# Optimization experiments

Hardware: AMD Instinct MI355X
Metric: run time of the kernel (lower is better)

## Reference

```python
import jax, jax.numpy as jnp
import numpy as np

N, E, IN_FEATS, D, H, DIST_DIM, NBOUND = 10000, 160000, 128, 64, 4, 32, 31

def setup_inputs() -> dict:
    key = jax.random.key(0)
    ks = jax.random.split(key, 16)
    gain = 5.0 / 3.0  # tanh gain
    def xavier(k, shape):
        # xavier_normal over the last two dims (fan_in, fan_out) as torch does per-slice
        fan_in, fan_out = shape[-2], shape[-1]
        std = gain * np.sqrt(2.0 / (fan_in + fan_out))
        return jax.random.normal(k, shape, dtype=jnp.float32) * std
    inp = {
        'feat': jax.random.normal(ks[0], (N, IN_FEATS), dtype=jnp.float32),
        'locations': jax.random.normal(ks[1], (N, 3), dtype=jnp.float32),
        'src': jax.random.randint(ks[2], (E,), 0, N),
        'dst': jax.random.randint(ks[3], (E,), 0, N),
        'inter_ids': jax.random.randint(ks[4], (E, H), 0, N),
        'W_fc': xavier(ks[5], (IN_FEATS, H * D)),
        'embed_table': jax.random.normal(ks[6], (NBOUND + 1, DIST_DIM), dtype=jnp.float32),
        'G': xavier(ks[7], (H, DIST_DIM, D)),
        'attn_fc1': xavier(ks[8], (H, 2 * D, D)),
        'attn_fc2': xavier(ks[9], (H, 2 * D, D)),
        'attn_fc3': xavier(ks[10], (H, 2 * D, D)),
        'attn_fc': xavier(ks[11], (H, 3 * D, D)),
        'attn_out': xavier(ks[12], (H, D, 1)),
        'boundaries': jnp.linspace(0.1, 3.1, NBOUND).astype(jnp.float32),
    }
    return inp


def reference(feat, locations, W_fc, embed_table, G, attn_fc1, attn_fc2, attn_fc3,
              attn_fc, attn_out, boundaries, src, dst, inter_ids):
    n = feat.shape[0]
    h = (feat @ W_fc).reshape(n, H, D)                      # [N,H,D]
    pos = locations                                          # [N,3]
    src_pos = pos[src]                                       # [E,3]
    dst_pos = pos[dst]                                       # [E,3]
    inter_pos = pos[inter_ids]                               # [E,H,3]
    h_src = h[src]                                           # [E,H,D]
    h_dst = h[dst]                                           # [E,H,D]
    head_idx = jnp.arange(H)[None, :]
    inter_h = h[inter_ids, head_idx, :]                      # [E,H,D] per-head gather

    e_count = src.shape[0]
    dist1 = jnp.broadcast_to(jnp.linalg.norm(dst_pos - src_pos, axis=-1)[:, None], (e_count, H))
    dist2 = jnp.linalg.norm(dst_pos[:, None, :] - inter_pos, axis=-1)   # [E,H]
    dist_ = jnp.linalg.norm(src_pos[:, None, :] - inter_pos, axis=-1)   # [E,H]

    def dist_embed(dist):
        idx = jnp.searchsorted(boundaries, dist, side='left')  # torch.bucketize(right=False)
        e = embed_table[idx]                                   # [E,H,DIST_DIM]
        return jnp.einsum('ehk,hkd->ehd', e, G)                # [E,H,D]

    de1 = dist_embed(dist1)
    de2 = dist_embed(dist2)
    de_ = dist_embed(dist_)

    d1 = jnp.einsum('ehk,hkd->ehd', jnp.concatenate([h_src, de1], axis=-1), attn_fc1)
    d2 = jnp.einsum('ehk,hkd->ehd', jnp.concatenate([inter_h, de2], axis=-1), attn_fc2)
    d3 = jnp.einsum('ehk,hkd->ehd', jnp.concatenate([h_dst, de_], axis=-1), attn_fc3)

    h_c = jnp.tanh(jnp.einsum('ehk,hkd->ehd', jnp.concatenate([d1, d2, d3], axis=-1), attn_fc))
    e_score = jnp.einsum('ehd,hdo->eho', h_c, attn_out)[..., 0]        # [E,H]

    # edge softmax grouped by destination node
    m = jax.ops.segment_max(e_score, dst, num_segments=n)              # [N,H]
    ex = jnp.exp(e_score - m[dst])
    den = jax.ops.segment_sum(ex, dst, num_segments=n)                 # [N,H]
    a = ex / den[dst]                                                  # [E,H]

    ft = jax.ops.segment_sum(a[:, :, None] * h_src, dst, num_segments=n)  # [N,H,D]
    rst = jnp.mean(ft, axis=1)                                          # merge='mean' -> [N,D]
    return rst
```

## Files before the change

### kernel.cpp

```cpp
#include <hip/hip_runtime.h>
#include <hip/hip_fp16.h>
#include <math.h>

#define N_NODES 10000
#define E_EDGES 160000
#define DMODEL 64
#define H 4
#define NBOUND 31
#define SLOTS 64
#define QREC 1024

typedef _Float16 half8 __attribute__((ext_vector_type(8)));
typedef float floatx4 __attribute__((ext_vector_type(4)));

__device__ __forceinline__ void mm4(const float* __restrict__ S, int aoff,
                                    int astride, int boff, int i0, int j,
                                    int Kdim, float o[4]) {
  float a0 = 0.f, a1 = 0.f, a2 = 0.f, a3 = 0.f;
  for (int t4 = 0; t4 < (Kdim >> 2); ++t4) {
    float4 f0 = *(const float4*)&S[aoff + (i0 + 0) * astride + t4 * 4];
    float4 f1 = *(const float4*)&S[aoff + (i0 + 1) * astride + t4 * 4];
    float4 f2 = *(const float4*)&S[aoff + (i0 + 2) * astride + t4 * 4];
    float4 f3 = *(const float4*)&S[aoff + (i0 + 3) * astride + t4 * 4];
    float b0 = S[boff + (t4 * 4 + 0) * 64 + j];
    float b1 = S[boff + (t4 * 4 + 1) * 64 + j];
    float b2 = S[boff + (t4 * 4 + 2) * 64 + j];
    float b3 = S[boff + (t4 * 4 + 3) * 64 + j];
    a0 += f0.x * b0 + f0.y * b1 + f0.z * b2 + f0.w * b3;
    a1 += f1.x * b0 + f1.y * b1 + f1.z * b2 + f1.w * b3;
    a2 += f2.x * b0 + f2.y * b1 + f2.z * b2 + f2.w * b3;
    a3 += f3.x * b0 + f3.y * b1 + f3.z * b2 + f3.w * b3;
  }
  o[0] = a0; o[1] = a1; o[2] = a2; o[3] = a3;
}

__device__ __forceinline__ int didx(const float* __restrict__ bnd2, float d) {
  int g = (int)(d * 10.0f);
  g = (g < 0) ? 0 : ((g > 31) ? 31 : g);
  g += (bnd2[g + 1] < d) ? 1 : 0;
  g -= (bnd2[g] >= d) ? 1 : 0;
  return g;
}

__global__ __launch_bounds__(512) void prep_kernel(
    const float* __restrict__ fc1, const float* __restrict__ fc2,
    const float* __restrict__ fc3, const float* __restrict__ fcc,
    const float* __restrict__ Wfc, const float* __restrict__ G,
    const float* __restrict__ emb, const float* __restrict__ pos,
    __half* __restrict__ bigWT, __half* __restrict__ U16,
    int* __restrict__ cnt, float4* __restrict__ pos4) {
  __shared__ __align__(16) float S[12288];
  int bi = blockIdx.x;
  int tid = threadIdx.x;
  if (bi >= 36) {
    int n = (bi - 36) * 512 + tid;
    if (n < N_NODES) {
      cnt[n] = 0;
      pos4[n] = make_float4(pos[n * 3], pos[n * 3 + 1], pos[n * 3 + 2], 0.f);
    }
    return;
  }
  int ca = bi / 12;
  int kh = bi % 12;
  int k = kh >> 2, h = kh & 3;
  const float* fck = (k == 0) ? fc1 : (k == 1) ? fc2 : fc3;
  fck += h * 128 * 64;
  const float* F = fcc + h * 192 * 64 + k * 64 * 64;
  int j = tid & 63, ig = tid >> 6;
  float o[4];
  if (ca < 2) {
    #pragma unroll
    for (int u = 0; u < 2; ++u) {
      ((float4*)S)[u * 512 + tid] = ((const float4*)F)[u * 512 + tid];
      ((float4*)(S + 4096))[u * 512 + tid] = ((const float4*)fck)[u * 512 + tid];
    }
    __syncthreads();
    #pragma unroll
    for (int rg = 0; rg < 2; ++rg) {
      int i0 = ig * 8 + rg * 4;
      mm4(S, 4096, 64, 0, i0, j, 64, o);
      S[8192 + (i0 + 0) * 64 + j] = o[0];
      S[8192 + (i0 + 1) * 64 + j] = o[1];
      S[8192 + (i0 + 2) * 64 + j] = o[2];
      S[8192 + (i0 + 3) * 64 + j] = o[3];
    }
    __syncthreads();
    int rbase = (ca == 0) ? 0 : 64;
    #pragma unroll
    for (int u = 0; u < 2; ++u) {
      int fi = u * 512 + tid;
      int i = fi >> 4, c4 = fi & 15;
      ((float4*)(S + 4096))[fi] =
          ((const float4*)(Wfc + (rbase + i) * 256 + h * 64))[c4];
    }
    __syncthreads();
    if (k == 0) {
      #pragma unroll
      for (int u = 0; u < 8; ++u) {
        int idx = u * 512 + tid;
        int i = idx >> 6, jj = idx & 63;
        bigWT[(h * 64 + jj) * 128 + rbase + i] = __float2half(S[4096 + idx]);
      }
    }
    #pragma unroll
    for (int rg = 0; rg < 2; ++rg) {
      int i0 = ig * 8 + rg * 4;
      mm4(S, 4096, 64, 8192, i0, j, 64, o);
      int rb = ((k + 1) * 256 + h * 64 + j) * 128 + rbase;
      bigWT[rb + i0 + 0] = __float2half(o[0]);
      bigWT[rb + i0 + 1] = __float2half(o[1]);
      bigWT[rb + i0 + 2] = __float2half(o[2]);
      bigWT[rb + i0 + 3] = __float2half(o[3]);
    }
    return;
  }
  #pragma unroll
  for (int u = 0; u < 2; ++u) {
    ((float4*)S)[u * 512 + tid] = ((const float4*)F)[u * 512 + tid];
    ((float4*)(S + 4096))[u * 512 + tid] =
        ((const float4*)(fck + 4096))[u * 512 + tid];
  }
  __syncthreads();
  #pragma unroll
  for (int rg = 0; rg < 2; ++rg) {
    int i0 = ig * 8 + rg * 4;
    mm4(S, 4096, 64, 0, i0, j, 64, o);
    S[8192 + (i0 + 0) * 64 + j] = o[0];
    S[8192 + (i0 + 1) * 64 + j] = o[1];
    S[8192 + (i0 + 2) * 64 + j] = o[2];
    S[8192 + (i0 + 3) * 64 + j] = o[3];
  }
  __syncthreads();
  ((float4*)S)[tid] = ((const float4*)(G + h * 2048))[tid];
  if (tid < 256) ((float4*)(S + 2048))[tid] = ((const float4*)emb)[tid];
  __syncthreads();
  {
    int i0 = ig * 4;
    mm4(S, 0, 64, 8192, i0, j, 64, o);
    S[3072 + (i0 + 0) * 64 + j] = o[0];
    S[3072 + (i0 + 1) * 64 + j] = o[1];
    S[3072 + (i0 + 2) * 64 + j] = o[2];
    S[3072 + (i0 + 3) * 64 + j] = o[3];
  }
  __syncthreads();
  {
    int i0 = ig * 4;
    mm4(S, 2048, 32, 3072, i0, j, 32, o);
    int base = k * 8192 + h * 2048;
    U16[base + (i0 + 0) * 64 + j] = __float2half(o[0]);
    U16[base + (i0 + 1) * 64 + j] = __float2half(o[1]);
    U16[base + (i0 + 2) * 64 + j] = __float2half(o[2]);
    U16[base + (i0 + 3) * 64 + j] = __float2half(o[3]);
  }
}

#define EROW 264
#define NEDGE_BLK 1250

__global__ __launch_bounds__(128) void gemm_edge_kernel(
    const float* __restrict__ feat, const __half* __restrict__ bigWT,
    __half* __restrict__ qall, const float4* __restrict__ pos4,
    const int* __restrict__ src, const int* __restrict__ dst,
    const int* __restrict__ inter, const float* __restrict__ boundaries,
    int* __restrict__ cnt, uint4* __restrict__ ebuf) {
  __shared__ __align__(16) __half Esm[2][16][EROW];
  __shared__ float Sb[48];
  int bi = blockIdx.x;
  int tid = threadIdx.x;
  if (bi < NEDGE_BLK) {
    if (tid < NBOUND) Sb[tid + 1] = boundaries[tid];
    if (tid == NBOUND) { Sb[0] = -INFINITY; Sb[32] = INFINITY; }
    __syncthreads();
    int e = bi * 128 + tid;
    int s = src[e], t = dst[e];
    int4 iv = *(const int4*)&inter[e * 4];
    int itarr[4] = {iv.x, iv.y, iv.z, iv.w};
    float4 sp = pos4[s];
    float4 tp = pos4[t];
    float dx = tp.x - sp.x, dy = tp.y - sp.y, dz = tp.z - sp.z;
    float dist1 = sqrtf(dx * dx + dy * dy + dz * dz);
    unsigned i1 = (unsigned)didx(Sb, dist1);
    unsigned w3 = 0, q20 = 0, q_0 = 0;
    #pragma unroll
    for (int hh = 0; hh < 4; ++hh) {
      float4 ip = pos4[itarr[hh]];
      float ax = tp.x - ip.x, ay = tp.y - ip.y, az = tp.z - ip.z;
      float dist2 = sqrtf(ax * ax + ay * ay + az * az);
      float bx = sp.x - ip.x, by = sp.y - ip.y, bz = sp.z - ip.z;
      float dist_ = sqrtf(bx * bx + by * by + bz * bz);
      unsigned idx2 = (unsigned)didx(Sb, dist2);
      unsigned idx_ = (unsigned)didx(Sb, dist_);
      if (hh == 0) { q20 = idx2; q_0 = idx_; }
      else w3 |= (idx2 | (idx_ << 5)) << ((hh - 1) * 10);
    }
    uint4 rec;
    rec.x = (unsigned)s | ((unsigned)itarr[0] << 16);
    rec.y = (unsigned)itarr[1] | ((unsigned)itarr[2] << 16);
    rec.z = (unsigned)itarr[3] | (i1 << 16) | (q20 << 21) | (q_0 << 26);
    rec.w = w3;
    int p = atomicAdd(&cnt[t], 1);
    if (p < SLOTS) ebuf[t * SLOTS + p] = rec;
    return;
  }
  int gi = bi - NEDGE_BLK;
  int bx = gi % 313, by = gi / 313;
  int wv = tid >> 6, l = tid & 63;
  int m0 = bx * 32 + wv * 16;
  int n0 = by * 256;
  int lm = l & 15, lk = (l >> 4) * 8;
  int arow = m0 + lm;
  if (arow >= N_NODES) arow = N_NODES - 1;
  const float* fp = feat + arow * 128 + lk;
  const _Float16* bp = (const _Float16*)bigWT + lk;
  half8 a[4];
  #pragma unroll
  for (int kt = 0; kt < 4; ++kt) {
    float4 u0 = *(const float4*)(fp + kt * 32);
    float4 u1 = *(const float4*)(fp + kt * 32 + 4);
    half8 t;
    t[0] = (_Float16)u0.x; t[1] = (_Float16)u0.y;
    t[2] = (_Float16)u0.z; t[3] = (_Float16)u0.w;
    t[4] = (_Float16)u1.x; t[5] = (_Float16)u1.y;
    t[6] = (_Float16)u1.z; t[7] = (_Float16)u1.w;
    a[kt] = t;
  }
  #pragma unroll
  for (int nt = 0; nt < 16; ++nt) {
    floatx4 acc = (floatx4){0.f, 0.f, 0.f, 0.f};
    #pragma unroll
    for (int kt = 0; kt < 4; ++kt) {
      half8 b = *(const half8*)(bp + (n0 + nt * 16 + lm) * 128 + kt * 32);
      acc = __builtin_amdgcn_mfma_f32_16x16x32_f16(a[kt], b, acc, 0, 0, 0);
    }
    int dd = nt * 16 + lm;
    #pragma unroll
    for (int r4 = 0; r4 < 4; ++r4)
      Esm[wv][(l >> 4) * 4 + r4][dd] = __float2half(acc[r4]);
  }
  __syncthreads();
  int row = l >> 2;
  int j0 = (l & 3) * 64;
  int m = m0 + row;
  if (m < N_NODES) {
    #pragma unroll
    for (int u = 0; u < 8; ++u) {
      uint4 v = *(const uint4*)&Esm[wv][row][j0 + u * 8];
      *(uint4*)&qall[m * QREC + by * 256 + j0 + u * 8] = v;
    }
  }
}

__device__ __forceinline__ float dpp_bfly_sum16(float v) {
  int x;
  x = __builtin_amdgcn_update_dpp(0, __float_as_int(v), 0xB1, 0xf, 0xf, true);
  v += __int_as_float(x);
  x = __builtin_amdgcn_update_dpp(0, __float_as_int(v), 0x4E, 0xf, 0xf, true);
  v += __int_as_float(x);
  x = __builtin_amdgcn_update_dpp(0, __float_as_int(v), 0x141, 0xf, 0xf, true);
  v += __int_as_float(x);
  x = __builtin_amdgcn_update_dpp(0, __float_as_int(v), 0x140, 0xf, 0xf, true);
  v += __int_as_float(x);
  return v;
}

union H4u { uint2 u; __half2 h[2]; };

__device__ __forceinline__ float tanh_dot(H4u A, H4u B, H4u C, H4u X, H4u Y,
                                          H4u Z, float4 a4) {
  __half2 z0 = __hadd2(__hadd2(A.h[0], B.h[0]), __hadd2(C.h[0], X.h[0]));
  z0 = __hadd2(z0, __hadd2(Y.h[0], Z.h[0]));
  __half2 z1 = __hadd2(__hadd2(A.h[1], B.h[1]), __hadd2(C.h[1], X.h[1]));
  z1 = __hadd2(z1, __hadd2(Y.h[1], Z.h[1]));
  float2 f0 = __half22float2(z0);
  float2 f1 = __half22float2(z1);
  const float K = 2.885390082f;
  float p0 = __builtin_amdgcn_exp2f(f0.x * K);
  float p1 = __builtin_amdgcn_exp2f(f0.y * K);
  float p2 = __builtin_amdgcn_exp2f(f1.x * K);
  float p3 = __builtin_amdgcn_exp2f(f1.y * K);
  float r0 = __builtin_amdgcn_rcpf(p0 + 1.0f);
  float r1 = __builtin_amdgcn_rcpf(p1 + 1.0f);
  float r2 = __builtin_amdgcn_rcpf(p2 + 1.0f);
  float r3 = __builtin_amdgcn_rcpf(p3 + 1.0f);
  float dot = a4.x * r0;
  dot = fmaf(a4.y, r1, dot);
  dot = fmaf(a4.z, r2, dot);
  dot = fmaf(a4.w, r3, dot);
  float asum = (a4.x + a4.y) + (a4.z + a4.w);
  return fmaf(-2.0f, dot, asum);
}

__device__ __forceinline__ float4 h4_to_f4(uint2 u) {
  union { uint2 ui; __half2 h[2]; } cc;
  cc.ui = u;
  float2 a = __half22float2(cc.h[0]);
  float2 b = __half22float2(cc.h[1]);
  return make_float4(a.x, a.y, b.x, b.y);
}

__device__ __forceinline__ void dec_rec(uint4 r, int h, int* s, int* it,
                                        unsigned* i1, unsigned* q2,
                                        unsigned* q_) {
  *s = (int)(r.x & 0xffff);
  *it = (h == 0) ? (int)(r.x >> 16)
      : (h == 1) ? (int)(r.y & 0xffff)
      : (h == 2) ? (int)(r.y >> 16) : (int)(r.z & 0xffff);
  *i1 = (r.z >> 16) & 31;
  if (h == 0) {
    *q2 = (r.z >> 21) & 31;
    *q_ = (r.z >> 26) & 31;
  } else {
    unsigned f = r.w >> ((h - 1) * 10);
    *q2 = f & 31;
    *q_ = (f >> 5) & 31;
  }
}

__global__ __launch_bounds__(256) void score_agg_kernel(
    const int* __restrict__ cnt, const uint4* __restrict__ ebuf,
    const __half* __restrict__ qall, const __half* __restrict__ U16,
    const float* __restrict__ aout, float* __restrict__ out) {
  __shared__ uint4 recs[SLOTS];
  __shared__ float4 sm_num[4][64];
  __shared__ float sm_den[4][4];
  int tid = threadIdx.x;
  int w = tid >> 6, lane = tid & 63;
  int h = lane >> 4, c = lane & 15;
  int n = blockIdx.x;
  int deg = cnt[n];
  if (deg > SLOTS) deg = SLOTS;
  if (tid < deg) recs[tid] = ebuf[n * SLOTS + tid];
  H4u C;
  C.u = *(const uint2*)(qall + n * QREC + 768 + h * 64 + c * 4);
  const float4 a4 = *((const float4*)(aout + h * 64) + c);
  __syncthreads();
  float4 num = make_float4(0.f, 0.f, 0.f, 0.f);
  float den = 0.f;
  int hc4 = h * 64 + c * 4;
  for (int i = w; i < deg; i += 8) {
    int iB = i + 4;
    int vB = (iB < deg);
    uint4 rA = recs[i];
    uint4 rB = recs[vB ? iB : i];
    int sA, itA, sB, itB;
    unsigned i1A, q2A, q_A, i1B, q2B, q_B;
    dec_rec(rA, h, &sA, &itA, &i1A, &q2A, &q_A);
    dec_rec(rB, h, &sB, &itB, &i1B, &q2B, &q_B);
    H4u A0, B0, X0, Y0, Z0, A1, B1, X1, Y1, Z1;
    uint2 hr0, hr1;
    hr0 = *(const uint2*)(qall + sA * QREC + hc4);
    A0.u = *(const uint2*)(qall + sA * QREC + 256 + hc4);
    B0.u = *(const uint2*)(qall + itA * QREC + 512 + hc4);
    X0.u = *(const uint2*)(U16 + (h * 32 + (int)i1A) * 64 + c * 4);
    Y0.u = *(const uint2*)(U16 + 8192 + (h * 32 + (int)q2A) * 64 + c * 4);
    Z0.u = *(const uint2*)(U16 + 16384 + (h * 32 + (int)q_A) * 64 + c * 4);
    hr1 = *(const uint2*)(qall + sB * QREC + hc4);
    A1.u = *(const uint2*)(qall + sB * QREC + 256 + hc4);
    B1.u = *(const uint2*)(qall + itB * QREC + 512 + hc4);
    X1.u = *(const uint2*)(U16 + (h * 32 + (int)i1B) * 64 + c * 4);
    Y1.u = *(const uint2*)(U16 + 8192 + (h * 32 + (int)q2B) * 64 + c * 4);
    Z1.u = *(const uint2*)(U16 + 16384 + (h * 32 + (int)q_B) * 64 + c * 4);
    float v0 = tanh_dot(A0, B0, C, X0, Y0, Z0, a4);
    float v1 = tanh_dot(A1, B1, C, X1, Y1, Z1, a4);
    v0 = dpp_bfly_sum16(v0);
    v1 = dpp_bfly_sum16(v1);
    float ex0 = __expf(v0);
    float ex1 = vB ? __expf(v1) : 0.f;
    float4 hv0 = h4_to_f4(hr0);
    float4 hv1 = h4_to_f4(hr1);
    num.x += ex0 * hv0.x + ex1 * hv1.x;
    num.y += ex0 * hv0.y + ex1 * hv1.y;
    num.z += ex0 * hv0.z + ex1 * hv1.z;
    num.w += ex0 * hv0.w + ex1 * hv1.w;
    den += ex0 + ex1;
  }
  sm_num[w][lane] = num;
  if (c == 0) sm_den[w][h] = den;
  __syncthreads();
  if (tid < 64) {
    float4 n0 = sm_num[0][lane], n1 = sm_num[1][lane];
    float4 n2 = sm_num[2][lane], n3 = sm_num[3][lane];
    float dt = sm_den[0][h] + sm_den[1][h] + sm_den[2][h] + sm_den[3][h];
    float4 t = make_float4(0.f, 0.f, 0.f, 0.f);
    if (deg > 0) {
      float inv = 1.0f / dt;
      t.x = (n0.x + n1.x + n2.x + n3.x) * inv;
      t.y = (n0.y + n1.y + n2.y + n3.y) * inv;
      t.z = (n0.z + n1.z + n2.z + n3.z) * inv;
      t.w = (n0.w + n1.w + n2.w + n3.w) * inv;
    }
    t.x += __shfl_xor(t.x, 16); t.y += __shfl_xor(t.y, 16);
    t.z += __shfl_xor(t.z, 16); t.w += __shfl_xor(t.w, 16);
    t.x += __shfl_xor(t.x, 32); t.y += __shfl_xor(t.y, 32);
    t.z += __shfl_xor(t.z, 32); t.w += __shfl_xor(t.w, 32);
    if (h == 0) {
      t.x *= 0.25f; t.y *= 0.25f; t.z *= 0.25f; t.w *= 0.25f;
      *(float4*)&out[n * 64 + c * 4] = t;
    }
  }
}

extern "C" void kernel_launch(void* const* d_in, const int* in_sizes, int n_in,
                              void* d_out, int out_size, void* d_ws,
                              size_t ws_size, hipStream_t stream) {
  const float* feat = (const float*)d_in[0];
  const float* loc = (const float*)d_in[1];
  const int* src = (const int*)d_in[2];
  const int* dst = (const int*)d_in[3];
  const int* inter = (const int*)d_in[4];
  const float* Wfc = (const float*)d_in[5];
  const float* emb = (const float*)d_in[6];
  const float* G = (const float*)d_in[7];
  const float* fc1 = (const float*)d_in[8];
  const float* fc2 = (const float*)d_in[9];
  const float* fc3 = (const float*)d_in[10];
  const float* fcc = (const float*)d_in[11];
  const float* aout = (const float*)d_in[12];
  const float* bnd = (const float*)d_in[13];
  float* out = (float*)d_out;

  __half* qall = (__half*)d_ws;
  __half* bigWT = qall + N_NODES * QREC;
  __half* U16 = bigWT + 1024 * 128;
  uint4* ebuf = (uint4*)(U16 + 3 * H * 2048);
  int* cnt = (int*)(ebuf + N_NODES * SLOTS);
  float4* pos4 = (float4*)(cnt + N_NODES);

  prep_kernel<<<56, 512, 0, stream>>>(fc1, fc2, fc3, fcc, Wfc, G, emb, loc,
                                      bigWT, U16, cnt, pos4);
  gemm_edge_kernel<<<2502, 128, 0, stream>>>(feat, bigWT, qall, pos4, src, dst,
                                             inter, bnd, cnt, ebuf);
  score_agg_kernel<<<N_NODES, 256, 0, stream>>>(cnt, ebuf, qall, U16, aout,
                                                out);
}
```

Measured before the change: 178.4 us.

## Split fused gemm/edge kernel into separate edge and GEMM launches with larger blocks

```diff
diff --git a/kernel.cpp b/kernel.cpp
--- a/kernel.cpp
+++ b/kernel.cpp
@@ -154,58 +154,63 @@
   }
 }
 
+__global__ __launch_bounds__(256) void edge_kernel(
+    const float4* __restrict__ pos4, const int* __restrict__ src,
+    const int* __restrict__ dst, const int* __restrict__ inter,
+    const float* __restrict__ boundaries, int* __restrict__ cnt,
+    uint4* __restrict__ ebuf) {
+  __shared__ float Sb[48];
+  int tid = threadIdx.x;
+  if (tid < NBOUND) Sb[tid + 1] = boundaries[tid];
+  if (tid == NBOUND) { Sb[0] = -INFINITY; Sb[32] = INFINITY; }
+  int e = blockIdx.x * 256 + tid;
+  int s = src[e], t = dst[e];
+  int p = atomicAdd(&cnt[t], 1);
+  int4 iv = *(const int4*)&inter[e * 4];
+  int itarr[4] = {iv.x, iv.y, iv.z, iv.w};
+  float4 sp = pos4[s];
+  float4 tp = pos4[t];
+  float4 ip0 = pos4[itarr[0]];
+  float4 ip1 = pos4[itarr[1]];
+  float4 ip2 = pos4[itarr[2]];
+  float4 ip3 = pos4[itarr[3]];
+  __syncthreads();
+  float dx = tp.x - sp.x, dy = tp.y - sp.y, dz = tp.z - sp.z;
+  float dist1 = sqrtf(dx * dx + dy * dy + dz * dz);
+  unsigned i1 = (unsigned)didx(Sb, dist1);
+  float4 ips[4] = {ip0, ip1, ip2, ip3};
+  unsigned w3 = 0, q20 = 0, q_0 = 0;
+  #pragma unroll
+  for (int hh = 0; hh < 4; ++hh) {
+    float4 ip = ips[hh];
+    float ax = tp.x - ip.x, ay = tp.y - ip.y, az = tp.z - ip.z;
+    float dist2 = sqrtf(ax * ax + ay * ay + az * az);
+    float bx = sp.x - ip.x, by = sp.y - ip.y, bz = sp.z - ip.z;
+    float dist_ = sqrtf(bx * bx + by * by + bz * bz);
+    unsigned idx2 = (unsigned)didx(Sb, dist2);
+    unsigned idx_ = (unsigned)didx(Sb, dist_);
+    if (hh == 0) { q20 = idx2; q_0 = idx_; }
+    else w3 |= (idx2 | (idx_ << 5)) << ((hh - 1) * 10);
+  }
+  uint4 rec;
+  rec.x = (unsigned)s | ((unsigned)itarr[0] << 16);
+  rec.y = (unsigned)itarr[1] | ((unsigned)itarr[2] << 16);
+  rec.z = (unsigned)itarr[3] | (i1 << 16) | (q20 << 21) | (q_0 << 26);
+  rec.w = w3;
+  if (p < SLOTS) ebuf[t * SLOTS + p] = rec;
+}
+
 #define EROW 264
-#define NEDGE_BLK 1250
-
-__global__ __launch_bounds__(128) void gemm_edge_kernel(
+
+__global__ __launch_bounds__(256) void gemm_kernel(
     const float* __restrict__ feat, const __half* __restrict__ bigWT,
-    __half* __restrict__ qall, const float4* __restrict__ pos4,
-    const int* __restrict__ src, const int* __restrict__ dst,
-    const int* __restrict__ inter, const float* __restrict__ boundaries,
-    int* __restrict__ cnt, uint4* __restrict__ ebuf) {
-  __shared__ __align__(16) __half Esm[2][16][EROW];
-  __shared__ float Sb[48];
+    __half* __restrict__ qall) {
+  __shared__ __align__(16) __half Esm[4][16][EROW];
   int bi = blockIdx.x;
   int tid = threadIdx.x;
-  if (bi < NEDGE_BLK) {
-    if (tid < NBOUND) Sb[tid + 1] = boundaries[tid];
-    if (tid == NBOUND) { Sb[0] = -INFINITY; Sb[32] = INFINITY; }
-    __syncthreads();
-    int e = bi * 128 + tid;
-    int s = src[e], t = dst[e];
-    int4 iv = *(const int4*)&inter[e * 4];
-    int itarr[4] = {iv.x, iv.y, iv.z, iv.w};
-    float4 sp = pos4[s];
-    float4 tp = pos4[t];
-    float dx = tp.x - sp.x, dy = tp.y - sp.y, dz = tp.z - sp.z;
-    float dist1 = sqrtf(dx * dx + dy * dy + dz * dz);
-    unsigned i1 = (unsigned)didx(Sb, dist1);
-    unsigned w3 = 0, q20 = 0, q_0 = 0;
-    #pragma unroll
-    for (int hh = 0; hh < 4; ++hh) {
-      float4 ip = pos4[itarr[hh]];
-      float ax = tp.x - ip.x, ay = tp.y - ip.y, az = tp.z - ip.z;
-      float dist2 = sqrtf(ax * ax + ay * ay + az * az);
-      float bx = sp.x - ip.x, by = sp.y - ip.y, bz = sp.z - ip.z;
-      float dist_ = sqrtf(bx * bx + by * by + bz * bz);
-      unsigned idx2 = (unsigned)didx(Sb, dist2);
-      unsigned idx_ = (unsigned)didx(Sb, dist_);
-      if (hh == 0) { q20 = idx2; q_0 = idx_; }
-      else w3 |= (idx2 | (idx_ << 5)) << ((hh - 1) * 10);
-    }
-    uint4 rec;
-    rec.x = (unsigned)s | ((unsigned)itarr[0] << 16);
-    rec.y = (unsigned)itarr[1] | ((unsigned)itarr[2] << 16);
-    rec.z = (unsigned)itarr[3] | (i1 << 16) | (q20 << 21) | (q_0 << 26);
-    rec.w = w3;
-    int p = atomicAdd(&cnt[t], 1);
-    if (p < SLOTS) ebuf[t * SLOTS + p] = rec;
-    return;
-  }
-  int gi = bi - NEDGE_BLK;
-  int bx = gi % 313, by = gi / 313;
+  int bx = bi % 157, by = bi / 157;
   int wv = tid >> 6, l = tid & 63;
-  int m0 = bx * 32 + wv * 16;
+  int m0 = bx * 64 + wv * 16;
   int n0 = by * 256;
   int lm = l & 15, lk = (l >> 4) * 8;
   int arow = m0 + lm;
@@ -428,8 +433,9 @@
 
   prep_kernel<<<56, 512, 0, stream>>>(fc1, fc2, fc3, fcc, Wfc, G, emb, loc,
                                       bigWT, U16, cnt, pos4);
-  gemm_edge_kernel<<<2502, 128, 0, stream>>>(feat, bigWT, qall, pos4, src, dst,
-                                             inter, bnd, cnt, ebuf);
+  edge_kernel<<<E_EDGES / 256, 256, 0, stream>>>(pos4, src, dst, inter, bnd,
+                                                 cnt, ebuf);
+  gemm_kernel<<<628, 256, 0, stream>>>(feat, bigWT, qall);
   score_agg_kernel<<<N_NODES, 256, 0, stream>>>(cnt, ebuf, qall, U16, aout,
                                                 out);
 }
```

After: 182.2 us. +2.1%, slower.
